# Kernel tuning notes

Measured on AMD Instinct MI355X. Metric: run time of the kernel, lower is better.

The kernel has to match this reference:

```python
import jax, jax.numpy as jnp
import numpy as np

B, F, C, O, M = 128, 4096, 32, 32, 9  # batch, num_fields, in_ch, out_ch, num_coeffs (moves incl. self)


def setup_inputs() -> dict:
    key = jax.random.key(0)
    k1, k2, k3, k4 = jax.random.split(key, 4)
    x = jax.random.normal(k1, (B, F, C), dtype=jnp.float32)
    # mask[m, f] = index of the source field feeding target field f via move m
    mask = jax.random.randint(k2, (M, F), 0, F, dtype=jnp.int32)
    init_std = 1.0 / (3.0 * np.sqrt(C * O))  # matches TruncatedNormal stddev in build()
    conv_coeffs = jax.random.normal(k3, (M, C, O), dtype=jnp.float32) * init_std
    # biases are zero-initialized in the original; use small random values so the
    # bias-add path is exercised numerically
    biases = jax.random.normal(k4, (F, O), dtype=jnp.float32) * 0.01
    return {"x": x, "mask": mask, "conv_coeffs": conv_coeffs, "biases": biases}


def reference(x, mask, conv_coeffs, biases):
    # ch_convolve_by_moves: gather source fields per move, per-move matmul, per-field bias.
    # gathered[b, m, f, c] = x[b, mask[m, f], c]
    gathered = jnp.take(x, mask, axis=1)              # [B, M, F, C]
    out = jnp.einsum('bmfc,mco->bfo', gathered, conv_coeffs)  # sum over moves and in-channels
    return out + biases                               # per-field bias broadcast over batch
```

## Files before the change

### kernel.cpp

```cpp
#include <hip/hip_runtime.h>


#define B_ 128
#define F_ 4096
#define C_ 32
#define O_ 32
#define M_ 9
#define T_ 18

typedef _Float16 halfx8 __attribute__((ext_vector_type(8)));
typedef float floatx4 __attribute__((ext_vector_type(4)));
typedef float floatx16 __attribute__((ext_vector_type(16)));

__global__ __launch_bounds__(256, 3) void fused_conv(
    const float* __restrict__ x, const int* __restrict__ mask,
    const float* __restrict__ coeffs, const float* __restrict__ biases,
    float* __restrict__ out)
{
    __shared__ _Float16 sw[T_ * 64 * 8];

    const int tid = threadIdx.x;
    for (int id = tid; id < T_ * 64; id += 256) {
        const int t  = id >> 6;
        const int L  = id & 63;
        const int m  = t >> 1;
        const int cb = 16 * (t & 1) + 8 * (L >> 5);
        const int oo = L & 31;
        halfx8 w;
#pragma unroll
        for (int jj = 0; jj < 8; ++jj)
            w[jj] = (_Float16)coeffs[(m * C_ + cb + jj) * O_ + oo];
        *reinterpret_cast<halfx8*>(&sw[id * 8]) = w;
    }
    __syncthreads();

    const int blk = blockIdx.x;
    const int p   = blk >> 10;
    const int xcd = blk & 7;
    const int ft  = (blk >> 3) & 127;
    const int b0  = (p * 8 + xcd) * 4;
    const int f0  = ft * 32;

    const int wave = tid >> 6;
    const int lane = tid & 63;
    const int h    = lane >> 5;
    const int row  = lane & 31;
    const int fi   = row >> 2;
    const int bp   = row & 3;
    const int o    = lane & 31;

    const int fw = f0 + wave * 8;
    const int f  = fw + fi;

    int sidx[M_];
#pragma unroll
    for (int m = 0; m < M_; ++m) sidx[m] = mask[m * F_ + f];

    const float* xrow = x + (size_t)(b0 + bp) * (F_ * C_) + 8 * h;

    halfx8 a[T_];
#pragma unroll
    for (int m = 0; m < M_; ++m) {
        const float* rp = xrow + (size_t)sidx[m] * C_;
        const floatx4 v0 = *reinterpret_cast<const floatx4*>(rp);
        const floatx4 v1 = *reinterpret_cast<const floatx4*>(rp + 4);
        const floatx4 v2 = *reinterpret_cast<const floatx4*>(rp + 16);
        const floatx4 v3 = *reinterpret_cast<const floatx4*>(rp + 20);
        halfx8 lo, hi;
#pragma unroll
        for (int jj = 0; jj < 4; ++jj) {
            lo[jj]     = (_Float16)v0[jj];
            lo[jj + 4] = (_Float16)v1[jj];
            hi[jj]     = (_Float16)v2[jj];
            hi[jj + 4] = (_Float16)v3[jj];
        }
        a[2 * m]     = lo;
        a[2 * m + 1] = hi;
    }

    floatx16 acc;
#pragma unroll
    for (int i = 0; i < 16; ++i) acc[i] = 0.0f;
#pragma unroll
    for (int t = 0; t < T_; ++t) {
        const halfx8 bwt = *reinterpret_cast<const halfx8*>(&sw[(t * 64 + lane) * 8]);
        acc = __builtin_amdgcn_mfma_f32_32x32x16_f16(a[t], bwt, acc, 0, 0, 0);
    }

    float bv[4];
#pragma unroll
    for (int q = 0; q < 4; ++q)
        bv[q] = biases[(size_t)(fw + 2 * q + h) * O_ + o];

#pragma unroll
    for (int r = 0; r < 16; ++r) {
        const int q   = r >> 2;
        const int obp = r & 3;
        const float v = acc[r] + bv[q];
        __builtin_nontemporal_store(
            v, &out[((size_t)(b0 + obp) * F_ + fw + 2 * q + h) * O_ + o]);
    }
}

extern "C" void kernel_launch(void* const* d_in, const int* in_sizes, int n_in,
                              void* d_out, int out_size, void* d_ws, size_t ws_size,
                              hipStream_t stream) {
    (void)in_sizes; (void)n_in; (void)d_ws; (void)ws_size; (void)out_size;
    fused_conv<<<4 * 8 * 128, 256, 0, stream>>>(
        (const float*)d_in[0], (const int*)d_in[1],
        (const float*)d_in[2], (const float*)d_in[3], (float*)d_out);
}
```

Before: 176.1 us.

## Stage gathered x rows through swizzled LDS with coalesced loads and software pipelining

Each lane now loads one 16-byte piece of a gathered source row, so eight lanes cover a full 128-byte field row with one instruction. The pieces are converted to fp16 and written into a per-wave, XOR-swizzled LDS buffer, then read back in the MFMA A-operand layout. The nine moves are split into three groups, and the global loads for the next group are issued before the MFMAs of the current group so load latency overlaps compute. This adds LDS write and read traffic and about 24KB of shared memory per block, which may limit occupancy. In exchange it removes the 18-register A-fragment array.

```diff
diff --git a/kernel.cpp b/kernel.cpp
--- a/kernel.cpp
+++ b/kernel.cpp
@@ -7,7 +7,12 @@
 #define O_ 32
 #define M_ 9
 #define T_ 18
+#define GM 3
+#define NG 3
+#define FB 32
+#define BB 4
 
+typedef _Float16 halfx4 __attribute__((ext_vector_type(4)));
 typedef _Float16 halfx8 __attribute__((ext_vector_type(8)));
 typedef float floatx4 __attribute__((ext_vector_type(4)));
 typedef float floatx16 __attribute__((ext_vector_type(16)));
@@ -18,8 +23,10 @@
     float* __restrict__ out)
 {
     __shared__ _Float16 sw[T_ * 64 * 8];
+    __shared__ _Float16 al[GM * FB * BB * C_];
 
     const int tid = threadIdx.x;
+
     for (int id = tid; id < T_ * 64; id += 256) {
         const int t  = id >> 6;
         const int L  = id & 63;
@@ -50,41 +57,93 @@
     const int o    = lane & 31;
 
     const int fw = f0 + wave * 8;
-    const int f  = fw + fi;
+
+    const int sf  = lane >> 3;
+    const int sc4 = (lane & 7) * 4;
 
     int sidx[M_];
 #pragma unroll
-    for (int m = 0; m < M_; ++m) sidx[m] = mask[m * F_ + f];
+    for (int m = 0; m < M_; ++m) sidx[m] = mask[m * F_ + fw + sf];
 
-    const float* xrow = x + (size_t)(b0 + bp) * (F_ * C_) + 8 * h;
+    const float* xbase = x + (size_t)b0 * (F_ * C_) + sc4;
 
-    halfx8 a[T_];
-#pragma unroll
-    for (int m = 0; m < M_; ++m) {
-        const float* rp = xrow + (size_t)sidx[m] * C_;
-        const floatx4 v0 = *reinterpret_cast<const floatx4*>(rp);
-        const floatx4 v1 = *reinterpret_cast<const floatx4*>(rp + 4);
-        const floatx4 v2 = *reinterpret_cast<const floatx4*>(rp + 16);
-        const floatx4 v3 = *reinterpret_cast<const floatx4*>(rp + 20);
-        halfx8 lo, hi;
-#pragma unroll
-        for (int jj = 0; jj < 4; ++jj) {
-            lo[jj]     = (_Float16)v0[jj];
-            lo[jj + 4] = (_Float16)v1[jj];
-            hi[jj]     = (_Float16)v2[jj];
-            hi[jj + 4] = (_Float16)v3[jj];
-        }
-        a[2 * m]     = lo;
-        a[2 * m + 1] = hi;
-    }
+    const int wbase = (wave * 8 + sf) * (BB * C_) + sc4;
+    const int rbase = (wave * 8 + fi) * (BB * C_) + bp * C_ + h * 8;
+    const int wswz  = sf << 3;
+    const int rswz  = fi << 3;
 
     floatx16 acc;
 #pragma unroll
     for (int i = 0; i < 16; ++i) acc[i] = 0.0f;
+
+    {
+        floatx4 stg[GM * BB];
 #pragma unroll
-    for (int t = 0; t < T_; ++t) {
-        const halfx8 bwt = *reinterpret_cast<const halfx8*>(&sw[(t * 64 + lane) * 8]);
-        acc = __builtin_amdgcn_mfma_f32_32x32x16_f16(a[t], bwt, acc, 0, 0, 0);
+        for (int ml = 0; ml < GM; ++ml)
+#pragma unroll
+            for (int q = 0; q < BB; ++q)
+                stg[ml * BB + q] = *reinterpret_cast<const floatx4*>(
+                    xbase + (size_t)q * (F_ * C_) + (size_t)sidx[ml] * C_);
+#pragma unroll
+        for (int ml = 0; ml < GM; ++ml)
+#pragma unroll
+            for (int q = 0; q < BB; ++q) {
+                halfx4 hv;
+#pragma unroll
+                for (int jj = 0; jj < 4; ++jj)
+                    hv[jj] = (_Float16)stg[ml * BB + q][jj];
+                const int hw = ((ml * FB) * (BB * C_) + wbase + q * C_) ^ wswz;
+                *reinterpret_cast<halfx4*>(&al[hw]) = hv;
+            }
+    }
+
+#pragma unroll
+    for (int g = 0; g < NG; ++g) {
+        floatx4 stg[GM * BB];
+        if (g < NG - 1) {
+#pragma unroll
+            for (int ml = 0; ml < GM; ++ml)
+#pragma unroll
+                for (int q = 0; q < BB; ++q)
+                    stg[ml * BB + q] = *reinterpret_cast<const floatx4*>(
+                        xbase + (size_t)q * (F_ * C_) +
+                        (size_t)sidx[(g + 1) * GM + ml] * C_);
+        }
+
+        halfx8 af[2 * GM];
+#pragma unroll
+        for (int ml = 0; ml < GM; ++ml)
+#pragma unroll
+            for (int k = 0; k < 2; ++k) {
+                const int hr = ((ml * FB) * (BB * C_) + rbase + k * 16) ^ rswz;
+                af[ml * 2 + k] = *reinterpret_cast<const halfx8*>(&al[hr]);
+            }
+
+#pragma unroll
+        for (int ml = 0; ml < GM; ++ml)
+#pragma unroll
+            for (int k = 0; k < 2; ++k) {
+                const int t = (g * GM + ml) * 2 + k;
+                const halfx8 bwt =
+                    *reinterpret_cast<const halfx8*>(&sw[(t * 64 + lane) * 8]);
+                acc = __builtin_amdgcn_mfma_f32_32x32x16_f16(
+                    af[ml * 2 + k], bwt, acc, 0, 0, 0);
+            }
+
+        if (g < NG - 1) {
+#pragma unroll
+            for (int ml = 0; ml < GM; ++ml)
+#pragma unroll
+                for (int q = 0; q < BB; ++q) {
+                    halfx4 hv;
+#pragma unroll
+                    for (int jj = 0; jj < 4; ++jj)
+                        hv[jj] = (_Float16)stg[ml * BB + q][jj];
+                    const int hw =
+                        ((ml * FB) * (BB * C_) + wbase + q * C_) ^ wswz;
+                    *reinterpret_cast<halfx4*>(&al[hw]) = hv;
+                }
+        }
     }
 
     float bv[4];
```

Result: faster. 144.9 us (-17.7%).

## Stage gathered rows through LDS with double-buffered register prefetch

Applied to the files above, without the earlier changes.

Each lane now loads a contiguous 16-byte chunk of gathered x rows, so one field row is read coalesced by 8 lanes instead of being read in strided 8-element pieces. The rows are converted to fp16 and written to a per-wave swizzled LDS tile, then read back in MFMA operand layout. Loads for later moves are issued into two alternating register sets while earlier moves are converted and multiplied, overlapping gather latency with compute. Occupancy bound is raised to 4 blocks. In exchange it adds LDS traffic and 16KB of LDS per block, and it relies on wave-local LDS ordering without an explicit barrier.

```diff
diff --git a/kernel.cpp b/kernel.cpp
--- a/kernel.cpp
+++ b/kernel.cpp
@@ -8,18 +8,57 @@
 #define M_ 9
 #define T_ 18
 
+typedef _Float16 halfx4 __attribute__((ext_vector_type(4)));
 typedef _Float16 halfx8 __attribute__((ext_vector_type(8)));
 typedef float floatx4 __attribute__((ext_vector_type(4)));
 typedef float floatx16 __attribute__((ext_vector_type(16)));
 
-__global__ __launch_bounds__(256, 3) void fused_conv(
+#define STAGE(SET, GB, NM)                                                  \
+  _Pragma("unroll")                                                         \
+  for (int ml = 0; ml < (NM); ++ml)                                         \
+    _Pragma("unroll")                                                       \
+    for (int q = 0; q < 4; ++q)                                             \
+      SET[ml * 4 + q] = *reinterpret_cast<const floatx4*>(                  \
+          xbase + (size_t)q * (F_ * C_) + (size_t)sidx[(GB) + ml] * C_);
+
+#define CVTWR(SET, NM)                                                      \
+  _Pragma("unroll")                                                         \
+  for (int ml = 0; ml < (NM); ++ml)                                         \
+    _Pragma("unroll")                                                       \
+    for (int q = 0; q < 4; ++q) {                                           \
+      halfx4 hv;                                                            \
+      _Pragma("unroll")                                                     \
+      for (int jj = 0; jj < 4; ++jj)                                        \
+        hv[jj] = (_Float16)SET[ml * 4 + q][jj];                             \
+      *reinterpret_cast<halfx4*>(                                           \
+          &al[wslot + ((ml * 4 + q) * 8 + sf) * 32 + ((cq * 4) ^ wkey)]) =  \
+          hv;                                                               \
+    }
+
+#define RDMM(GB, NM)                                                        \
+  _Pragma("unroll")                                                         \
+  for (int ml = 0; ml < (NM); ++ml)                                         \
+    _Pragma("unroll")                                                       \
+    for (int k = 0; k < 2; ++k) {                                           \
+      const halfx8 af = *reinterpret_cast<const halfx8*>(                   \
+          &al[wslot + ((ml * 4 + bp) * 8 + fi) * 32 +                       \
+              ((k * 16 + h * 8) ^ rkey)]);                                  \
+      const int t = ((GB) + ml) * 2 + k;                                    \
+      const halfx8 bwt =                                                    \
+          *reinterpret_cast<const halfx8*>(&sw[(t * 64 + lane) * 8]);       \
+      acc = __builtin_amdgcn_mfma_f32_32x32x16_f16(af, bwt, acc, 0, 0, 0);  \
+    }
+
+__global__ __launch_bounds__(256, 4) void fused_conv(
     const float* __restrict__ x, const int* __restrict__ mask,
     const float* __restrict__ coeffs, const float* __restrict__ biases,
     float* __restrict__ out)
 {
     __shared__ _Float16 sw[T_ * 64 * 8];
+    __shared__ _Float16 al[4 * 2048];
 
     const int tid = threadIdx.x;
+
     for (int id = tid; id < T_ * 64; id += 256) {
         const int t  = id >> 6;
         const int L  = id & 63;
@@ -50,42 +89,33 @@
     const int o    = lane & 31;
 
     const int fw = f0 + wave * 8;
-    const int f  = fw + fi;
+
+    const int sf = lane >> 3;
+    const int cq = lane & 7;
+
+    const int wslot = wave * 2048;
+    const int wkey  = (sf & 3) << 3;
+    const int rkey  = (fi & 3) << 3;
 
     int sidx[M_];
 #pragma unroll
-    for (int m = 0; m < M_; ++m) sidx[m] = mask[m * F_ + f];
+    for (int m = 0; m < M_; ++m) sidx[m] = mask[m * F_ + fw + sf];
 
-    const float* xrow = x + (size_t)(b0 + bp) * (F_ * C_) + 8 * h;
-
-    halfx8 a[T_];
-#pragma unroll
-    for (int m = 0; m < M_; ++m) {
-        const float* rp = xrow + (size_t)sidx[m] * C_;
-        const floatx4 v0 = *reinterpret_cast<const floatx4*>(rp);
-        const floatx4 v1 = *reinterpret_cast<const floatx4*>(rp + 4);
-        const floatx4 v2 = *reinterpret_cast<const floatx4*>(rp + 16);
-        const floatx4 v3 = *reinterpret_cast<const floatx4*>(rp + 20);
-        halfx8 lo, hi;
-#pragma unroll
-        for (int jj = 0; jj < 4; ++jj) {
-            lo[jj]     = (_Float16)v0[jj];
-            lo[jj + 4] = (_Float16)v1[jj];
-            hi[jj]     = (_Float16)v2[jj];
-            hi[jj + 4] = (_Float16)v3[jj];
-        }
-        a[2 * m]     = lo;
-        a[2 * m + 1] = hi;
-    }
+    const float* xbase = x + (size_t)b0 * (F_ * C_) + cq * 4;
 
     floatx16 acc;
 #pragma unroll
     for (int i = 0; i < 16; ++i) acc[i] = 0.0f;
-#pragma unroll
-    for (int t = 0; t < T_; ++t) {
-        const halfx8 bwt = *reinterpret_cast<const halfx8*>(&sw[(t * 64 + lane) * 8]);
-        acc = __builtin_amdgcn_mfma_f32_32x32x16_f16(a[t], bwt, acc, 0, 0, 0);
-    }
+
+    floatx4 sA[8], sB[8];
+    STAGE(sA, 0, 2);
+    STAGE(sB, 2, 2);
+
+    CVTWR(sA, 2);  STAGE(sA, 4, 2);  RDMM(0, 2);
+    CVTWR(sB, 2);  STAGE(sB, 6, 2);  RDMM(2, 2);
+    CVTWR(sA, 2);  STAGE(sA, 8, 1);  RDMM(4, 2);
+    CVTWR(sB, 2);                    RDMM(6, 2);
+    CVTWR(sA, 1);                    RDMM(8, 1);
 
     float bv[4];
 #pragma unroll
```

Result: faster. 141.9 us (-19.4%).

## Pre-convert x to fp16 field-major workspace before gather GEMM pass

Applied to the files above, without the earlier changes.

Adds a first pass that converts x to fp16 once and writes it into a field-major workspace layout, with the batch group and channel half interleaved so each lane's MFMA operand is one contiguous 16-byte load. The GEMM pass then gathers half-size rows directly instead of loading fp32 and converting 9 times per element, which cuts gather traffic. It also reverses the batch-group order so that recently written workspace data may still be in cache. The cost is an extra kernel launch plus a full write and re-read of the fp16 copy of x. A scalar fallback kernel runs when the workspace is too small.

```diff
diff --git a/kernel.cpp b/kernel.cpp
--- a/kernel.cpp
+++ b/kernel.cpp
@@ -8,18 +8,47 @@
 #define M_ 9
 #define T_ 18
 
+typedef _Float16 halfx4 __attribute__((ext_vector_type(4)));
 typedef _Float16 halfx8 __attribute__((ext_vector_type(8)));
 typedef float floatx4 __attribute__((ext_vector_type(4)));
 typedef float floatx16 __attribute__((ext_vector_type(16)));
 
-__global__ __launch_bounds__(256, 3) void fused_conv(
-    const float* __restrict__ x, const int* __restrict__ mask,
+__global__ __launch_bounds__(256) void pass1_cvt(
+    const float* __restrict__ x, _Float16* __restrict__ xh)
+{
+    const int blk = blockIdx.x;
+    const int xcd = blk & 7;
+    const int ft  = (blk >> 3) & 127;
+    const int p   = blk >> 10;
+    const int b0  = (p * 8 + xcd) * 4;
+    const int f0  = ft * 32;
+    const int fl  = threadIdx.x >> 3;
+    const int c4  = (threadIdx.x & 7) * 4;
+    const int k   = c4 >> 4;
+    const int h   = (c4 >> 3) & 1;
+    const int j0  = c4 & 7;
+    _Float16* dst = xh + (size_t)(f0 + fl) * (B_ * C_) + (b0 >> 2) * 128
+                    + (k * 8 + h * 4) * 8 + j0;
+#pragma unroll
+    for (int q = 0; q < 4; ++q) {
+        const floatx4 v = __builtin_nontemporal_load(
+            reinterpret_cast<const floatx4*>(
+                x + ((size_t)(b0 + q) * F_ + f0 + fl) * C_ + c4));
+        halfx4 hv;
+#pragma unroll
+        for (int jj = 0; jj < 4; ++jj) hv[jj] = (_Float16)v[jj];
+        *reinterpret_cast<halfx4*>(dst + q * 8) = hv;
+    }
+}
+
+__global__ __launch_bounds__(256, 3) void pass2_gemm(
+    const _Float16* __restrict__ xh, const int* __restrict__ mask,
     const float* __restrict__ coeffs, const float* __restrict__ biases,
     float* __restrict__ out)
 {
     __shared__ _Float16 sw[T_ * 64 * 8];
+    const int tid = threadIdx.x;
 
-    const int tid = threadIdx.x;
     for (int id = tid; id < T_ * 64; id += 256) {
         const int t  = id >> 6;
         const int L  = id & 63;
@@ -35,9 +64,9 @@
     __syncthreads();
 
     const int blk = blockIdx.x;
-    const int p   = blk >> 10;
     const int xcd = blk & 7;
     const int ft  = (blk >> 3) & 127;
+    const int p   = 3 - (blk >> 10);
     const int b0  = (p * 8 + xcd) * 4;
     const int f0  = ft * 32;
 
@@ -48,34 +77,21 @@
     const int fi   = row >> 2;
     const int bp   = row & 3;
     const int o    = lane & 31;
-
-    const int fw = f0 + wave * 8;
-    const int f  = fw + fi;
+    const int fw   = f0 + wave * 8;
+    const int f    = fw + fi;
 
     int sidx[M_];
 #pragma unroll
     for (int m = 0; m < M_; ++m) sidx[m] = mask[m * F_ + f];
 
-    const float* xrow = x + (size_t)(b0 + bp) * (F_ * C_) + 8 * h;
+    const _Float16* xb = xh + (b0 >> 2) * 128 + (h * 4 + bp) * 8;
 
     halfx8 a[T_];
 #pragma unroll
     for (int m = 0; m < M_; ++m) {
-        const float* rp = xrow + (size_t)sidx[m] * C_;
-        const floatx4 v0 = *reinterpret_cast<const floatx4*>(rp);
-        const floatx4 v1 = *reinterpret_cast<const floatx4*>(rp + 4);
-        const floatx4 v2 = *reinterpret_cast<const floatx4*>(rp + 16);
-        const floatx4 v3 = *reinterpret_cast<const floatx4*>(rp + 20);
-        halfx8 lo, hi;
-#pragma unroll
-        for (int jj = 0; jj < 4; ++jj) {
-            lo[jj]     = (_Float16)v0[jj];
-            lo[jj + 4] = (_Float16)v1[jj];
-            hi[jj]     = (_Float16)v2[jj];
-            hi[jj + 4] = (_Float16)v3[jj];
-        }
-        a[2 * m]     = lo;
-        a[2 * m + 1] = hi;
+        const _Float16* rp = xb + (size_t)sidx[m] * (B_ * C_);
+        a[2 * m]     = *reinterpret_cast<const halfx8*>(rp);
+        a[2 * m + 1] = *reinterpret_cast<const halfx8*>(rp + 64);
     }
 
     floatx16 acc;
@@ -102,11 +118,42 @@
     }
 }
 
+__global__ __launch_bounds__(256) void fallback_kernel(
+    const float* __restrict__ x, const int* __restrict__ mask,
+    const float* __restrict__ coeffs, const float* __restrict__ biases,
+    float* __restrict__ out)
+{
+    int gid = blockIdx.x * 256 + threadIdx.x;
+    int o = gid & (O_ - 1);
+    int f = (gid >> 5) & (F_ - 1);
+    int b = gid >> 17;
+    float acc = biases[f * O_ + o];
+    for (int m = 0; m < M_; ++m) {
+        int s = mask[m * F_ + f];
+        const float* xr = x + ((size_t)b * F_ + s) * C_;
+        const float* wr = coeffs + (m * C_) * O_ + o;
+#pragma unroll
+        for (int c = 0; c < C_; ++c)
+            acc += xr[c] * wr[c * O_];
+    }
+    out[gid] = acc;
+}
+
 extern "C" void kernel_launch(void* const* d_in, const int* in_sizes, int n_in,
                               void* d_out, int out_size, void* d_ws, size_t ws_size,
                               hipStream_t stream) {
-    (void)in_sizes; (void)n_in; (void)d_ws; (void)ws_size; (void)out_size;
-    fused_conv<<<4 * 8 * 128, 256, 0, stream>>>(
-        (const float*)d_in[0], (const int*)d_in[1],
-        (const float*)d_in[2], (const float*)d_in[3], (float*)d_out);
+    const float* x      = (const float*)d_in[0];
+    const int*   mask   = (const int*)d_in[1];
+    const float* coeffs = (const float*)d_in[2];
+    const float* biases = (const float*)d_in[3];
+    float* out = (float*)d_out;
+
+    const size_t need = (size_t)F_ * B_ * C_ * sizeof(_Float16);
+    if (ws_size >= need) {
+        _Float16* xh = (_Float16*)d_ws;
+        pass1_cvt<<<4 * 8 * 128, 256, 0, stream>>>(x, xh);
+        pass2_gemm<<<4 * 8 * 128, 256, 0, stream>>>(xh, mask, coeffs, biases, out);
+    } else {
+        fallback_kernel<<<(B_ * F_ * O_) / 256, 256, 0, stream>>>(x, mask, coeffs, biases, out);
+    }
 }
```

Result: faster. 145.8 us (-17.2%).
